# Optimization experiments

Measured on AMD Instinct MI355X. Metric: run time of the kernel, lower is better.

## Reference

```python
import jax, jax.numpy as jnp
import numpy as np

BITS = 4
MAXQ = (1 << BITS) - 1  # 15
PACK_BITS = 32
GROUP_SIZE = 128


def setup_inputs() -> dict:
    key = jax.random.key(0)
    k1, k2, k3, k4, k5 = jax.random.split(key, 5)
    in_f, out_f, tokens = 4096, 11008, 8192
    pack_factor = PACK_BITS // BITS  # 8
    n_groups = in_f // GROUP_SIZE  # 32
    x = jax.random.normal(k1, (tokens, in_f), dtype=jnp.float32)
    qweight = jax.random.randint(k2, (in_f // pack_factor, out_f), 0, 2147483647, dtype=jnp.int32)
    qzeros = jax.random.randint(k3, (n_groups, out_f // pack_factor), 0, 2147483647, dtype=jnp.int32)
    scales = jax.random.uniform(k4, (n_groups, out_f), dtype=jnp.float32) * 0.01 + 1e-3
    bias = jax.random.normal(k5, (out_f,), dtype=jnp.float32)
    g_idx = (jnp.arange(in_f, dtype=jnp.int32) // GROUP_SIZE).astype(jnp.int32)
    return {"x": x, "qweight": qweight, "qzeros": qzeros, "scales": scales, "bias": bias, "g_idx": g_idx}


def _dequantize(qweight, qzeros, scales, g_idx, in_features):
    # wf = [0, 4, 8, ..., 28]
    shifts = jnp.arange(0, PACK_BITS, BITS, dtype=jnp.int32)
    # unpack zeros: [G, out/8] -> [G, out/8, 8] -> [G, out]
    zeros = (qzeros[:, :, None] >> shifts[None, None, :]) & MAXQ
    zeros = zeros.reshape(scales.shape)
    # unpack weight: [in/8, out] -> [in/8, 8, out] -> [in, out]
    w = (qweight[:, None, :] >> shifts[None, :, None]) & MAXQ
    w = w.reshape(-1, scales.shape[1])[:in_features]
    # dequant: scales[g_idx] * (w - zeros[g_idx])
    return scales[g_idx] * (w - zeros[g_idx]).astype(scales.dtype)


def reference(x, qweight, qzeros, scales, bias, g_idx):
    W = _dequantize(qweight, qzeros, scales, g_idx, x.shape[1])  # [in, out]
    return x @ W + bias
```

## Files before the change

kernel.cpp:

```cpp
#include <hip/hip_runtime.h>
#include <hip/hip_bf16.h>

typedef __attribute__((ext_vector_type(8))) short short8;
typedef __attribute__((ext_vector_type(4))) float f32x4;
typedef __attribute__((ext_vector_type(4))) unsigned int uint4v;

#define BM 256
#define BN 256
#define BK 64

__device__ __forceinline__ void gl_lds16(const __hip_bfloat16* g, __hip_bfloat16* l) {
  __builtin_amdgcn_global_load_lds((const __attribute__((address_space(1))) void*)g,
                                   (__attribute__((address_space(3))) void*)l,
                                   16, 0, 0);
}

__global__ void dequant_kernel(const int* __restrict__ qweight,
                               const int* __restrict__ qzeros,
                               const float* __restrict__ scales,
                               __hip_bfloat16* __restrict__ wp, int N, int K) {
  const int n = blockIdx.x * 256 + threadIdx.x;
  const int kc = blockIdx.y;
  const int g = kc >> 4;
  const float s = scales[(size_t)g * N + n];
  const int zq = qzeros[(size_t)g * (N >> 3) + (n >> 3)];
  const float c = s * (float)((zq >> ((n & 7) * 4)) & 15);
  const int q = qweight[(size_t)kc * N + n];
  __hip_bfloat16 v[8];
#pragma unroll
  for (int j = 0; j < 8; j++)
    v[j] = __float2bfloat16(fmaf(s, (float)((q >> (4 * j)) & 15), -c));
  ((uint4v*)wp)[(size_t)kc * N + n] = *(const uint4v*)v;
}

__global__ void cvtx_kernel(const float* __restrict__ x,
                            __hip_bfloat16* __restrict__ xp, int M, int K) {
  __shared__ __hip_bfloat16 tile[64 * 64];
  const int t = threadIdx.x;
  const int m0 = blockIdx.x * 64, k0 = blockIdx.y * 64;
  const int mr = t >> 2, cq = t & 3;
  const float4* src = (const float4*)(x + (size_t)(m0 + mr) * K + k0 + cq * 16);
  const float4 a = src[0], b = src[1], c = src[2], d = src[3];
  __hip_bfloat16 v[16];
  v[0] = __float2bfloat16(a.x);  v[1] = __float2bfloat16(a.y);
  v[2] = __float2bfloat16(a.z);  v[3] = __float2bfloat16(a.w);
  v[4] = __float2bfloat16(b.x);  v[5] = __float2bfloat16(b.y);
  v[6] = __float2bfloat16(b.z);  v[7] = __float2bfloat16(b.w);
  v[8] = __float2bfloat16(c.x);  v[9] = __float2bfloat16(c.y);
  v[10] = __float2bfloat16(c.z); v[11] = __float2bfloat16(c.w);
  v[12] = __float2bfloat16(d.x); v[13] = __float2bfloat16(d.y);
  v[14] = __float2bfloat16(d.z); v[15] = __float2bfloat16(d.w);
  *(uint4v*)&tile[((cq * 2 + 0) * 64 + mr) * 8] = *(const uint4v*)&v[0];
  *(uint4v*)&tile[((cq * 2 + 1) * 64 + mr) * 8] = *(const uint4v*)&v[8];
  __syncthreads();
#pragma unroll
  for (int j = 0; j < 2; j++) {
    const int s = j * 256 + t;
    const int c8 = s >> 6, m = s & 63;
    ((uint4v*)xp)[(size_t)((k0 >> 3) + c8) * M + m0 + m] = *(const uint4v*)&tile[s * 8];
  }
}

__global__ __launch_bounds__(512, 2) void gemm_kernel(
    const __hip_bfloat16* __restrict__ Xp,
    const __hip_bfloat16* __restrict__ Wp,
    const float* __restrict__ bias,
    float* __restrict__ C, int M, int N, int K) {
  __shared__ __hip_bfloat16 As[2][8 * 256 * 8];
  __shared__ __hip_bfloat16 Bs[2][8 * 256 * 8];
  const int tid = threadIdx.x;
  const int m0 = blockIdx.x * BM;
  const int n0 = blockIdx.y * BN;
  const int wid = tid >> 6, ln = tid & 63;
  const int wmoff = (wid >> 2) * 128;
  const int wnoff = (wid & 3) * 64;
  const int lr = ln & 15, q4 = ln >> 4;

  f32x4 acc[8][4] = {};
  const int NT = K >> 6;

  auto stageA = [&](int t, int hs, int buf) {
#pragma unroll
    for (int i = 0; i < 2; ++i) {
      const int s = i * 512 + tid;
      const int c8 = (hs << 2) + (s >> 8);
      const int row = s & 255;
      gl_lds16(Xp + ((size_t)(t * 8 + c8) * M + m0 + row) * 8,
               &As[buf][(c8 * 256 + row) * 8]);
    }
  };
  auto stageB = [&](int t, int hs, int buf) {
#pragma unroll
    for (int i = 0; i < 2; ++i) {
      const int s = i * 512 + tid;
      const int c8 = (hs << 2) + (s >> 8);
      const int row = s & 255;
      gl_lds16(Wp + ((size_t)(t * 8 + c8) * N + n0 + row) * 8,
               &Bs[buf][(c8 * 256 + row) * 8]);
    }
  };

  stageA(0, 0, 0); stageA(0, 1, 0); stageB(0, 0, 0); stageB(0, 1, 0);
  if (NT > 1) {
    stageA(1, 0, 1); stageB(1, 0, 1); stageA(1, 1, 1);
    asm volatile("s_waitcnt vmcnt(6)" ::: "memory");
  } else {
    asm volatile("s_waitcnt vmcnt(0)" ::: "memory");
  }
  __builtin_amdgcn_s_barrier();

  short8 af[8], bf[2];

  for (int t = 0; t < NT; ++t) {
    const int cur = t & 1, nxt = cur ^ 1;
    const __hip_bfloat16* Ac = As[cur];
    const __hip_bfloat16* Bc = Bs[cur];

#pragma unroll
    for (int mf = 0; mf < 8; ++mf)
      af[mf] = *(const short8*)&Ac[(q4 * 256 + wmoff + mf * 16 + lr) * 8];
#pragma unroll
    for (int j = 0; j < 2; ++j)
      bf[j] = *(const short8*)&Bc[(q4 * 256 + wnoff + j * 16 + lr) * 8];
    if (t + 1 < NT) stageB(t + 1, 1, nxt);
    __builtin_amdgcn_s_barrier();
    asm volatile("s_waitcnt lgkmcnt(0)" ::: "memory");
    __builtin_amdgcn_s_setprio(1);
#pragma unroll
    for (int mf = 0; mf < 8; ++mf) {
      acc[mf][0] = __builtin_amdgcn_mfma_f32_16x16x32_bf16(af[mf], bf[0], acc[mf][0], 0, 0, 0);
      acc[mf][1] = __builtin_amdgcn_mfma_f32_16x16x32_bf16(af[mf], bf[1], acc[mf][1], 0, 0, 0);
    }
    __builtin_amdgcn_s_setprio(0);
    __builtin_amdgcn_s_barrier();

#pragma unroll
    for (int j = 0; j < 2; ++j)
      bf[j] = *(const short8*)&Bc[(q4 * 256 + wnoff + (2 + j) * 16 + lr) * 8];
    if (t + 2 < NT) stageA(t + 2, 0, cur);
    __builtin_amdgcn_s_barrier();
    asm volatile("s_waitcnt lgkmcnt(0)" ::: "memory");
    __builtin_amdgcn_s_setprio(1);
#pragma unroll
    for (int mf = 0; mf < 8; ++mf) {
      acc[mf][2] = __builtin_amdgcn_mfma_f32_16x16x32_bf16(af[mf], bf[0], acc[mf][2], 0, 0, 0);
      acc[mf][3] = __builtin_amdgcn_mfma_f32_16x16x32_bf16(af[mf], bf[1], acc[mf][3], 0, 0, 0);
    }
    __builtin_amdgcn_s_setprio(0);
    __builtin_amdgcn_s_barrier();

#pragma unroll
    for (int mf = 0; mf < 8; ++mf)
      af[mf] = *(const short8*)&Ac[((4 + q4) * 256 + wmoff + mf * 16 + lr) * 8];
#pragma unroll
    for (int j = 0; j < 2; ++j)
      bf[j] = *(const short8*)&Bc[((4 + q4) * 256 + wnoff + j * 16 + lr) * 8];
    if (t + 2 < NT) stageB(t + 2, 0, cur);
    __builtin_amdgcn_s_barrier();
    asm volatile("s_waitcnt lgkmcnt(0)" ::: "memory");
    __builtin_amdgcn_s_setprio(1);
#pragma unroll
    for (int mf = 0; mf < 8; ++mf) {
      acc[mf][0] = __builtin_amdgcn_mfma_f32_16x16x32_bf16(af[mf], bf[0], acc[mf][0], 0, 0, 0);
      acc[mf][1] = __builtin_amdgcn_mfma_f32_16x16x32_bf16(af[mf], bf[1], acc[mf][1], 0, 0, 0);
    }
    __builtin_amdgcn_s_setprio(0);
    __builtin_amdgcn_s_barrier();

#pragma unroll
    for (int j = 0; j < 2; ++j)
      bf[j] = *(const short8*)&Bc[((4 + q4) * 256 + wnoff + (2 + j) * 16 + lr) * 8];
    if (t + 2 < NT) stageA(t + 2, 1, cur);
    if (t == NT - 2) asm volatile("s_waitcnt vmcnt(0)" ::: "memory");
    else             asm volatile("s_waitcnt vmcnt(6)" ::: "memory");
    __builtin_amdgcn_s_barrier();
    asm volatile("s_waitcnt lgkmcnt(0)" ::: "memory");
    __builtin_amdgcn_s_setprio(1);
#pragma unroll
    for (int mf = 0; mf < 8; ++mf) {
      acc[mf][2] = __builtin_amdgcn_mfma_f32_16x16x32_bf16(af[mf], bf[0], acc[mf][2], 0, 0, 0);
      acc[mf][3] = __builtin_amdgcn_mfma_f32_16x16x32_bf16(af[mf], bf[1], acc[mf][3], 0, 0, 0);
    }
    __builtin_amdgcn_s_setprio(0);
    __builtin_amdgcn_s_barrier();
  }

  const int cr = m0 + wmoff + q4 * 4;
  const int cc = n0 + wnoff + lr;
#pragma unroll
  for (int nf = 0; nf < 4; ++nf) {
    const float bv = bias[cc + nf * 16];
#pragma unroll
    for (int mf = 0; mf < 8; ++mf) {
#pragma unroll
      for (int r = 0; r < 4; ++r) {
        C[(size_t)(cr + mf * 16 + r) * N + cc + nf * 16] = acc[mf][nf][r] + bv;
      }
    }
  }
}

__global__ void naive_kernel(const float* __restrict__ x, const int* __restrict__ qweight,
                             const int* __restrict__ qzeros, const float* __restrict__ scales,
                             const float* __restrict__ bias, const int* __restrict__ g_idx,
                             float* __restrict__ out, int in_f, int out_f) {
  const int n = blockIdx.x * blockDim.x + threadIdx.x;
  if (n >= out_f) return;
  const int m = blockIdx.y;
  const float* xr = x + (size_t)m * in_f;
  float acc = 0.f;
  for (int kk = 0; kk < (in_f >> 3); kk++) {
    const int q = qweight[(size_t)kk * out_f + n];
    const int g = g_idx[kk * 8];
    const float s = scales[(size_t)g * out_f + n];
    const int z = (qzeros[(size_t)g * (out_f >> 3) + (n >> 3)] >> ((n & 7) * 4)) & 15;
    float part = 0.f;
#pragma unroll
    for (int j = 0; j < 8; j++)
      part += xr[kk * 8 + j] * (float)(((q >> (4 * j)) & 15) - z);
    acc += s * part;
  }
  out[(size_t)m * out_f + n] = acc + bias[n];
}

extern "C" void kernel_launch(void* const* d_in, const int* in_sizes, int n_in,
                              void* d_out, int out_size, void* d_ws, size_t ws_size,
                              hipStream_t stream) {
  const float* x = (const float*)d_in[0];
  const int* qweight = (const int*)d_in[1];
  const int* qzeros = (const int*)d_in[2];
  const float* scales = (const float*)d_in[3];
  const float* bias = (const float*)d_in[4];
  const int* g_idx = (const int*)d_in[5];
  float* out = (float*)d_out;

  const int out_f = in_sizes[4];
  const int in_f = in_sizes[5];
  const int tokens = in_sizes[0] / in_f;

  const size_t need_w = (size_t)in_f * out_f * sizeof(__hip_bfloat16);
  const size_t need_x = (size_t)tokens * in_f * sizeof(__hip_bfloat16);

  if (ws_size >= need_w + need_x && (in_f % 128) == 0 && (out_f % 256) == 0 &&
      (tokens % 256) == 0) {
    __hip_bfloat16* wp = (__hip_bfloat16*)d_ws;
    __hip_bfloat16* xp = (__hip_bfloat16*)((char*)d_ws + need_w);
    dequant_kernel<<<dim3(out_f / 256, in_f / 8), 256, 0, stream>>>(
        qweight, qzeros, scales, wp, out_f, in_f);
    cvtx_kernel<<<dim3(tokens / 64, in_f / 64), 256, 0, stream>>>(x, xp, tokens, in_f);
    gemm_kernel<<<dim3(tokens / BM, out_f / BN), 512, 0, stream>>>(
        xp, wp, bias, out, tokens, out_f, in_f);
  } else {
    naive_kernel<<<dim3((out_f + 255) / 256, tokens), 256, 0, stream>>>(
        x, qweight, qzeros, scales, bias, g_idx, out, in_f, out_f);
  }
}
```

Measured before the change: 1.198 ms.

## Merge prep kernels and reorder GEMM inner loop into 2x2 quadrant MFMA phases

Combines the weight dequant and activation bf16 conversion into one launch that dispatches on block index, removing one kernel launch and the gap between the two. Restructures the GEMM inner loop so each phase computes a 4x2 fragment quadrant over both k-halves, loading A/B fragments per quadrant instead of per k-half. It also moves both stageA global loads to the final phase. This changes register pressure, the LDS read pattern and how loads overlap with MFMA, and the last phase drops its lgkmcnt wait since it reuses fragments already in registers.

```diff
diff --git a/kernel.cpp b/kernel.cpp
--- a/kernel.cpp
+++ b/kernel.cpp
@@ -15,49 +15,55 @@
                                    16, 0, 0);
 }
 
-__global__ void dequant_kernel(const int* __restrict__ qweight,
-                               const int* __restrict__ qzeros,
-                               const float* __restrict__ scales,
-                               __hip_bfloat16* __restrict__ wp, int N, int K) {
-  const int n = blockIdx.x * 256 + threadIdx.x;
-  const int kc = blockIdx.y;
-  const int g = kc >> 4;
-  const float s = scales[(size_t)g * N + n];
-  const int zq = qzeros[(size_t)g * (N >> 3) + (n >> 3)];
-  const float c = s * (float)((zq >> ((n & 7) * 4)) & 15);
-  const int q = qweight[(size_t)kc * N + n];
-  __hip_bfloat16 v[8];
-#pragma unroll
-  for (int j = 0; j < 8; j++)
-    v[j] = __float2bfloat16(fmaf(s, (float)((q >> (4 * j)) & 15), -c));
-  ((uint4v*)wp)[(size_t)kc * N + n] = *(const uint4v*)v;
-}
-
-__global__ void cvtx_kernel(const float* __restrict__ x,
-                            __hip_bfloat16* __restrict__ xp, int M, int K) {
+__global__ void prep_kernel(const int* __restrict__ qweight,
+                            const int* __restrict__ qzeros,
+                            const float* __restrict__ scales,
+                            __hip_bfloat16* __restrict__ wp,
+                            const float* __restrict__ x,
+                            __hip_bfloat16* __restrict__ xp,
+                            int N, int K, int M, int nDeq) {
   __shared__ __hip_bfloat16 tile[64 * 64];
-  const int t = threadIdx.x;
-  const int m0 = blockIdx.x * 64, k0 = blockIdx.y * 64;
-  const int mr = t >> 2, cq = t & 3;
-  const float4* src = (const float4*)(x + (size_t)(m0 + mr) * K + k0 + cq * 16);
-  const float4 a = src[0], b = src[1], c = src[2], d = src[3];
-  __hip_bfloat16 v[16];
-  v[0] = __float2bfloat16(a.x);  v[1] = __float2bfloat16(a.y);
-  v[2] = __float2bfloat16(a.z);  v[3] = __float2bfloat16(a.w);
-  v[4] = __float2bfloat16(b.x);  v[5] = __float2bfloat16(b.y);
-  v[6] = __float2bfloat16(b.z);  v[7] = __float2bfloat16(b.w);
-  v[8] = __float2bfloat16(c.x);  v[9] = __float2bfloat16(c.y);
-  v[10] = __float2bfloat16(c.z); v[11] = __float2bfloat16(c.w);
-  v[12] = __float2bfloat16(d.x); v[13] = __float2bfloat16(d.y);
-  v[14] = __float2bfloat16(d.z); v[15] = __float2bfloat16(d.w);
-  *(uint4v*)&tile[((cq * 2 + 0) * 64 + mr) * 8] = *(const uint4v*)&v[0];
-  *(uint4v*)&tile[((cq * 2 + 1) * 64 + mr) * 8] = *(const uint4v*)&v[8];
-  __syncthreads();
-#pragma unroll
-  for (int j = 0; j < 2; j++) {
-    const int s = j * 256 + t;
-    const int c8 = s >> 6, m = s & 63;
-    ((uint4v*)xp)[(size_t)((k0 >> 3) + c8) * M + m0 + m] = *(const uint4v*)&tile[s * 8];
+  const int id = blockIdx.x;
+  if (id < nDeq) {
+    const int nb = N >> 8;
+    const int n = (id % nb) * 256 + threadIdx.x;
+    const int kc = id / nb;
+    const int g = kc >> 4;
+    const float s = scales[(size_t)g * N + n];
+    const int zq = qzeros[(size_t)g * (N >> 3) + (n >> 3)];
+    const float c = s * (float)((zq >> ((n & 7) * 4)) & 15);
+    const int q = qweight[(size_t)kc * N + n];
+    __hip_bfloat16 v[8];
+#pragma unroll
+    for (int j = 0; j < 8; j++)
+      v[j] = __float2bfloat16(fmaf(s, (float)((q >> (4 * j)) & 15), -c));
+    ((uint4v*)wp)[(size_t)kc * N + n] = *(const uint4v*)v;
+  } else {
+    const int id2 = id - nDeq;
+    const int mb = M >> 6;
+    const int m0 = (id2 % mb) * 64, k0 = (id2 / mb) * 64;
+    const int t = threadIdx.x;
+    const int mr = t >> 2, cq = t & 3;
+    const float4* src = (const float4*)(x + (size_t)(m0 + mr) * K + k0 + cq * 16);
+    const float4 a = src[0], b = src[1], c = src[2], d = src[3];
+    __hip_bfloat16 v[16];
+    v[0] = __float2bfloat16(a.x);  v[1] = __float2bfloat16(a.y);
+    v[2] = __float2bfloat16(a.z);  v[3] = __float2bfloat16(a.w);
+    v[4] = __float2bfloat16(b.x);  v[5] = __float2bfloat16(b.y);
+    v[6] = __float2bfloat16(b.z);  v[7] = __float2bfloat16(b.w);
+    v[8] = __float2bfloat16(c.x);  v[9] = __float2bfloat16(c.y);
+    v[10] = __float2bfloat16(c.z); v[11] = __float2bfloat16(c.w);
+    v[12] = __float2bfloat16(d.x); v[13] = __float2bfloat16(d.y);
+    v[14] = __float2bfloat16(d.z); v[15] = __float2bfloat16(d.w);
+    *(uint4v*)&tile[((cq * 2 + 0) * 64 + mr) * 8] = *(const uint4v*)&v[0];
+    *(uint4v*)&tile[((cq * 2 + 1) * 64 + mr) * 8] = *(const uint4v*)&v[8];
+    __syncthreads();
+#pragma unroll
+    for (int j = 0; j < 2; j++) {
+      const int s = j * 256 + t;
+      const int c8 = s >> 6, m = s & 63;
+      ((uint4v*)xp)[(size_t)((k0 >> 3) + c8) * M + m0 + m] = *(const uint4v*)&tile[s * 8];
+    }
   }
 }
 
@@ -109,7 +115,7 @@
   }
   __builtin_amdgcn_s_barrier();
 
-  short8 af[8], bf[2];
+  short8 a[2][4], b0[2][2], b1[2][2];
 
   for (int t = 0; t < NT; ++t) {
     const int cur = t & 1, nxt = cur ^ 1;
@@ -117,70 +123,77 @@
     const __hip_bfloat16* Bc = Bs[cur];
 
 #pragma unroll
-    for (int mf = 0; mf < 8; ++mf)
-      af[mf] = *(const short8*)&Ac[(q4 * 256 + wmoff + mf * 16 + lr) * 8];
-#pragma unroll
-    for (int j = 0; j < 2; ++j)
-      bf[j] = *(const short8*)&Bc[(q4 * 256 + wnoff + j * 16 + lr) * 8];
+    for (int ks = 0; ks < 2; ++ks) {
+#pragma unroll
+      for (int mf = 0; mf < 4; ++mf)
+        a[ks][mf] = *(const short8*)&Ac[((ks * 4 + q4) * 256 + wmoff + mf * 16 + lr) * 8];
+#pragma unroll
+      for (int nf = 0; nf < 2; ++nf)
+        b0[ks][nf] = *(const short8*)&Bc[((ks * 4 + q4) * 256 + wnoff + nf * 16 + lr) * 8];
+    }
     if (t + 1 < NT) stageB(t + 1, 1, nxt);
     __builtin_amdgcn_s_barrier();
     asm volatile("s_waitcnt lgkmcnt(0)" ::: "memory");
     __builtin_amdgcn_s_setprio(1);
 #pragma unroll
-    for (int mf = 0; mf < 8; ++mf) {
-      acc[mf][0] = __builtin_amdgcn_mfma_f32_16x16x32_bf16(af[mf], bf[0], acc[mf][0], 0, 0, 0);
-      acc[mf][1] = __builtin_amdgcn_mfma_f32_16x16x32_bf16(af[mf], bf[1], acc[mf][1], 0, 0, 0);
-    }
-    __builtin_amdgcn_s_setprio(0);
-    __builtin_amdgcn_s_barrier();
-
-#pragma unroll
-    for (int j = 0; j < 2; ++j)
-      bf[j] = *(const short8*)&Bc[(q4 * 256 + wnoff + (2 + j) * 16 + lr) * 8];
-    if (t + 2 < NT) stageA(t + 2, 0, cur);
+    for (int mf = 0; mf < 4; ++mf)
+#pragma unroll
+      for (int nf = 0; nf < 2; ++nf) {
+        acc[mf][nf] = __builtin_amdgcn_mfma_f32_16x16x32_bf16(a[0][mf], b0[0][nf], acc[mf][nf], 0, 0, 0);
+        acc[mf][nf] = __builtin_amdgcn_mfma_f32_16x16x32_bf16(a[1][mf], b0[1][nf], acc[mf][nf], 0, 0, 0);
+      }
+    __builtin_amdgcn_s_setprio(0);
+    __builtin_amdgcn_s_barrier();
+
+#pragma unroll
+    for (int ks = 0; ks < 2; ++ks)
+#pragma unroll
+      for (int nf = 0; nf < 2; ++nf)
+        b1[ks][nf] = *(const short8*)&Bc[((ks * 4 + q4) * 256 + wnoff + 32 + nf * 16 + lr) * 8];
     __builtin_amdgcn_s_barrier();
     asm volatile("s_waitcnt lgkmcnt(0)" ::: "memory");
     __builtin_amdgcn_s_setprio(1);
 #pragma unroll
-    for (int mf = 0; mf < 8; ++mf) {
-      acc[mf][2] = __builtin_amdgcn_mfma_f32_16x16x32_bf16(af[mf], bf[0], acc[mf][2], 0, 0, 0);
-      acc[mf][3] = __builtin_amdgcn_mfma_f32_16x16x32_bf16(af[mf], bf[1], acc[mf][3], 0, 0, 0);
-    }
-    __builtin_amdgcn_s_setprio(0);
-    __builtin_amdgcn_s_barrier();
-
-#pragma unroll
-    for (int mf = 0; mf < 8; ++mf)
-      af[mf] = *(const short8*)&Ac[((4 + q4) * 256 + wmoff + mf * 16 + lr) * 8];
-#pragma unroll
-    for (int j = 0; j < 2; ++j)
-      bf[j] = *(const short8*)&Bc[((4 + q4) * 256 + wnoff + j * 16 + lr) * 8];
+    for (int mf = 0; mf < 4; ++mf)
+#pragma unroll
+      for (int nf = 0; nf < 2; ++nf) {
+        acc[mf][2 + nf] = __builtin_amdgcn_mfma_f32_16x16x32_bf16(a[0][mf], b1[0][nf], acc[mf][2 + nf], 0, 0, 0);
+        acc[mf][2 + nf] = __builtin_amdgcn_mfma_f32_16x16x32_bf16(a[1][mf], b1[1][nf], acc[mf][2 + nf], 0, 0, 0);
+      }
+    __builtin_amdgcn_s_setprio(0);
+    __builtin_amdgcn_s_barrier();
+
+#pragma unroll
+    for (int ks = 0; ks < 2; ++ks)
+#pragma unroll
+      for (int mf = 0; mf < 4; ++mf)
+        a[ks][mf] = *(const short8*)&Ac[((ks * 4 + q4) * 256 + wmoff + 64 + mf * 16 + lr) * 8];
     if (t + 2 < NT) stageB(t + 2, 0, cur);
     __builtin_amdgcn_s_barrier();
     asm volatile("s_waitcnt lgkmcnt(0)" ::: "memory");
     __builtin_amdgcn_s_setprio(1);
 #pragma unroll
-    for (int mf = 0; mf < 8; ++mf) {
-      acc[mf][0] = __builtin_amdgcn_mfma_f32_16x16x32_bf16(af[mf], bf[0], acc[mf][0], 0, 0, 0);
-      acc[mf][1] = __builtin_amdgcn_mfma_f32_16x16x32_bf16(af[mf], bf[1], acc[mf][1], 0, 0, 0);
-    }
-    __builtin_amdgcn_s_setprio(0);
-    __builtin_amdgcn_s_barrier();
-
-#pragma unroll
-    for (int j = 0; j < 2; ++j)
-      bf[j] = *(const short8*)&Bc[((4 + q4) * 256 + wnoff + (2 + j) * 16 + lr) * 8];
-    if (t + 2 < NT) stageA(t + 2, 1, cur);
+    for (int mf = 0; mf < 4; ++mf)
+#pragma unroll
+      for (int nf = 0; nf < 2; ++nf) {
+        acc[4 + mf][2 + nf] = __builtin_amdgcn_mfma_f32_16x16x32_bf16(a[0][mf], b1[0][nf], acc[4 + mf][2 + nf], 0, 0, 0);
+        acc[4 + mf][2 + nf] = __builtin_amdgcn_mfma_f32_16x16x32_bf16(a[1][mf], b1[1][nf], acc[4 + mf][2 + nf], 0, 0, 0);
+      }
+    __builtin_amdgcn_s_setprio(0);
+    __builtin_amdgcn_s_barrier();
+
+    if (t + 2 < NT) { stageA(t + 2, 0, cur); stageA(t + 2, 1, cur); }
     if (t == NT - 2) asm volatile("s_waitcnt vmcnt(0)" ::: "memory");
     else             asm volatile("s_waitcnt vmcnt(6)" ::: "memory");
     __builtin_amdgcn_s_barrier();
-    asm volatile("s_waitcnt lgkmcnt(0)" ::: "memory");
-    __builtin_amdgcn_s_setprio(1);
-#pragma unroll
-    for (int mf = 0; mf < 8; ++mf) {
-      acc[mf][2] = __builtin_amdgcn_mfma_f32_16x16x32_bf16(af[mf], bf[0], acc[mf][2], 0, 0, 0);
-      acc[mf][3] = __builtin_amdgcn_mfma_f32_16x16x32_bf16(af[mf], bf[1], acc[mf][3], 0, 0, 0);
-    }
+    __builtin_amdgcn_s_setprio(1);
+#pragma unroll
+    for (int mf = 0; mf < 4; ++mf)
+#pragma unroll
+      for (int nf = 0; nf < 2; ++nf) {
+        acc[4 + mf][nf] = __builtin_amdgcn_mfma_f32_16x16x32_bf16(a[0][mf], b0[0][nf], acc[4 + mf][nf], 0, 0, 0);
+        acc[4 + mf][nf] = __builtin_amdgcn_mfma_f32_16x16x32_bf16(a[1][mf], b0[1][nf], acc[4 + mf][nf], 0, 0, 0);
+      }
     __builtin_amdgcn_s_setprio(0);
     __builtin_amdgcn_s_barrier();
   }
@@ -245,9 +258,10 @@
       (tokens % 256) == 0) {
     __hip_bfloat16* wp = (__hip_bfloat16*)d_ws;
     __hip_bfloat16* xp = (__hip_bfloat16*)((char*)d_ws + need_w);
-    dequant_kernel<<<dim3(out_f / 256, in_f / 8), 256, 0, stream>>>(
-        qweight, qzeros, scales, wp, out_f, in_f);
-    cvtx_kernel<<<dim3(tokens / 64, in_f / 64), 256, 0, stream>>>(x, xp, tokens, in_f);
+    const int nDeq = (out_f >> 8) * (in_f >> 3);
+    const int nCvt = (tokens >> 6) * (in_f >> 6);
+    prep_kernel<<<dim3(nDeq + nCvt), 256, 0, stream>>>(
+        qweight, qzeros, scales, wp, x, xp, out_f, in_f, tokens, nDeq);
     gemm_kernel<<<dim3(tokens / BM, out_f / BN), 512, 0, stream>>>(
         xp, wp, bias, out, tokens, out_f, in_f);
   } else {
```

Measured after the change: 1.222 ms. Within noise of the previous version (+1.9%).
